# Kernel tuning notes

Hardware: AMD Instinct MI355X
Metric: run time of the kernel (lower is better)

Reference implementation:

```python
import jax, jax.numpy as jnp
import numpy as np

N_NODES = 100000


def gcn_conv(x, W, b, src, dst, n):
    # PyG GCNConv: linear transform, add self-loops, symmetric degree normalization,
    # scatter-add aggregation from src -> dst, then bias.
    h = x @ W  # [N, F_out]
    loop = jnp.arange(n, dtype=src.dtype)
    s = jnp.concatenate([src, loop])  # sources incl. self-loops
    d = jnp.concatenate([dst, loop])  # targets incl. self-loops
    deg = jax.ops.segment_sum(jnp.ones_like(d, dtype=h.dtype), d, num_segments=n)
    dinv = jnp.where(deg > 0, jax.lax.rsqrt(deg), 0.0)
    norm = dinv[s] * dinv[d]  # [E+N]
    msg = h[s] * norm[:, None]  # gather + scale
    out = jax.ops.segment_sum(msg, d, num_segments=n)  # scatter-add
    return out + b


def setup_inputs() -> dict:
    key = jax.random.key(0)
    k1, k2, k3, k4 = jax.random.split(key, 4)
    n, e = N_NODES, 1600000
    z = jax.random.normal(k1, (n, 64), dtype=jnp.float32)
    edge_index = jax.random.randint(k2, (2, e), 0, n, dtype=jnp.int64)
    # Glorot-ish init for weights, zero bias (PyG default bias init is zeros)
    W1 = jax.random.normal(k3, (64, 128), dtype=jnp.float32) * (1.0 / np.sqrt(64))
    b1 = jnp.zeros((128,), dtype=jnp.float32)
    W2 = jax.random.normal(k4, (128, 64), dtype=jnp.float32) * (1.0 / np.sqrt(128))
    b2 = jnp.zeros((64,), dtype=jnp.float32)
    return {"z": z, "edge_index": edge_index, "W1": W1, "b1": b1, "W2": W2, "b2": b2}


def reference(z, edge_index, W1, b1, W2, b2):
    n = z.shape[0]
    src, dst = edge_index[0], edge_index[1]
    h = gcn_conv(z, W1, b1, src, dst, n)
    h = jax.nn.relu(h)
    x_hat = gcn_conv(h, W2, b2, src, dst, n)
    return x_hat
```

## Files before the change

### kernel.cpp

```cpp
#include <hip/hip_runtime.h>
#include <hip/hip_bf16.h>


#define WAVE 64
#define BSHIFT 8
#define NPB 256
#define CAP 5120
#define CH 4096
#define NBMAX 512

typedef __attribute__((ext_vector_type(8))) short bf16x8;
typedef __attribute__((ext_vector_type(4))) float f32x4;

__device__ inline float bf16_to_f32(unsigned short h) {
    return __uint_as_float(((unsigned int)h) << 16);
}
__device__ inline unsigned short f32_to_bf16(float f) {
    unsigned int x = __float_as_uint(f);
    return (unsigned short)((x + 0x7FFFu + ((x >> 16) & 1u)) >> 16);
}

__global__ void prep(const float* __restrict__ W1, const float* __restrict__ W2,
                     unsigned short* __restrict__ W1t, unsigned short* __restrict__ W2t,
                     int* __restrict__ bcursor, int NB)
{
    int i = blockIdx.x * blockDim.x + threadIdx.x;
    if (i < NB) bcursor[i] = 0;
    if (i < 128 * 64) {
        int n = i >> 6, k = i & 63;
        W1t[i] = f32_to_bf16(W1[k * 128 + n]);
    }
    if (i < 64 * 128) {
        int n = i >> 7, k = i & 127;
        W2t[i] = f32_to_bf16(W2[k * 64 + n]);
    }
}

__global__ __launch_bounds__(256) void bin_edges(
        const int* __restrict__ src, const int* __restrict__ dst,
        int* __restrict__ bcursor, int2* __restrict__ ebuf, int E, int NB)
{
    __shared__ int hist[NBMAX];
    __shared__ int cur[NBMAX];
    const int t  = threadIdx.x;
    const int e0 = blockIdx.x * CH;

    for (int b = t; b < NB; b += 256) hist[b] = 0;
    __syncthreads();

#pragma unroll
    for (int j = 0; j < CH / 256; ++j) {
        int e = e0 + j * 256 + t;
        if (e < E) atomicAdd(&hist[dst[e] >> BSHIFT], 1);
    }
    __syncthreads();

    for (int b = t; b < NB; b += 256) {
        int c = hist[b];
        cur[b] = (c > 0) ? atomicAdd(&bcursor[b], c) : 0;
    }
    __syncthreads();

#pragma unroll
    for (int j = 0; j < CH / 256; ++j) {
        int e = e0 + j * 256 + t;
        if (e < E) {
            int s = src[e], d = dst[e];
            int b = d >> BSHIFT;
            int pos = atomicAdd(&cur[b], 1);
            ebuf[(size_t)b * CAP + pos] = make_int2(s, d);
        }
    }
}

__global__ __launch_bounds__(256) void build_csr(
        const int2* __restrict__ ebuf, const int* __restrict__ bcursor,
        const float* __restrict__ z, float* __restrict__ dinv,
        int* __restrict__ rbeg, int* __restrict__ rend,
        int* __restrict__ csr, unsigned short* __restrict__ u, int N)
{
    __shared__ int   h[NPB];
    __shared__ int   tmp[NPB];
    __shared__ float sdv[NPB];
    const int t   = threadIdx.x;
    const int b   = blockIdx.x;
    const int n0  = b << BSHIFT;
    const int cnt = bcursor[b];
    const size_t base = (size_t)b * CAP;

    h[t] = 0;
    __syncthreads();

    for (int i = t; i < cnt; i += 256)
        atomicAdd(&h[ebuf[base + i].y - n0], 1);
    __syncthreads();

    int deg = h[t];
    tmp[t] = deg;
    __syncthreads();
    for (int off = 1; off < 256; off <<= 1) {
        int x = (t >= off) ? tmp[t - off] : 0;
        __syncthreads();
        tmp[t] += x;
        __syncthreads();
    }
    int st = tmp[t] - deg;

    int node = n0 + t;
    float di = rsqrtf((float)deg + 1.0f);
    sdv[t] = di;
    if (node < N) {
        dinv[node] = di;
        rbeg[node] = (int)base + st;
        rend[node] = (int)base + st + deg;
    }
    h[t] = st;
    __syncthreads();

    for (int i = t; i < cnt; i += 256) {
        int2 e = ebuf[base + i];
        int p = atomicAdd(&h[e.y - n0], 1);
        csr[base + p] = e.x;
    }

    const int nloc = (N - n0 < NPB) ? (N - n0) : NPB;
    for (int i = t; i < nloc * 16; i += 256) {
        int r = i >> 4, kq = i & 15;
        float d2 = sdv[r];
        float4 v = ((const float4*)(z + (size_t)(n0 + r) * 64))[kq];
        ushort4 o;
        o.x = f32_to_bf16(v.x * d2);
        o.y = f32_to_bf16(v.y * d2);
        o.z = f32_to_bf16(v.z * d2);
        o.w = f32_to_bf16(v.w * d2);
        ((ushort4*)(u + (size_t)(n0 + r) * 64))[kq] = o;
    }
}

template<bool POST>
__global__ __launch_bounds__(256) void aggregate64_bf16(
        const unsigned short* __restrict__ hs, const int* __restrict__ rbeg,
        const int* __restrict__ rend, const int* __restrict__ csr,
        const float* __restrict__ dinv, const float* __restrict__ b,
        void* __restrict__ out_, int N)
{
    int node = (int)((blockIdx.x * (size_t)blockDim.x + threadIdx.x) >> 6);
    int lane = threadIdx.x & 63;
    if (node >= N) return;
    node = __builtin_amdgcn_readfirstlane(node);

    const int beg = rbeg[node];
    const int end = rend[node];

    float acc = bf16_to_f32(hs[(size_t)node * 64 + lane]);

    int e = beg;
    for (; e + 16 <= end; e += 16) {
        int s[16];
#pragma unroll
        for (int j = 0; j < 16; ++j) s[j] = csr[e + j];
        float v[16];
#pragma unroll
        for (int j = 0; j < 16; ++j) v[j] = bf16_to_f32(hs[(size_t)s[j] * 64 + lane]);
        float t0 = ((v[0] + v[1]) + (v[2] + v[3])) + ((v[4] + v[5]) + (v[6] + v[7]));
        float t1 = ((v[8] + v[9]) + (v[10] + v[11])) + ((v[12] + v[13]) + (v[14] + v[15]));
        acc += t0 + t1;
    }
    for (; e + 4 <= end; e += 4) {
        int s0 = csr[e+0], s1 = csr[e+1], s2 = csr[e+2], s3 = csr[e+3];
        float v0 = bf16_to_f32(hs[(size_t)s0 * 64 + lane]);
        float v1 = bf16_to_f32(hs[(size_t)s1 * 64 + lane]);
        float v2 = bf16_to_f32(hs[(size_t)s2 * 64 + lane]);
        float v3 = bf16_to_f32(hs[(size_t)s3 * 64 + lane]);
        acc += (v0 + v1) + (v2 + v3);
    }
    for (; e < end; ++e)
        acc += bf16_to_f32(hs[(size_t)csr[e] * 64 + lane]);

    if (POST) {
        float o = dinv[node] * acc + b[lane];
        ((float*)out_)[(size_t)node * 64 + lane] = o;
    } else {
        ((unsigned short*)out_)[(size_t)node * 64 + lane] = f32_to_bf16(acc);
    }
}

#define TILE 32
#define W1T_ST 72
#define W2T_ST 136
#define A_ST   72
#define X1_ST  136

__global__ __launch_bounds__(256) void gemm12_mfma(
        const unsigned short* __restrict__ agg1,
        const unsigned short* __restrict__ W1t,
        const float* __restrict__ b1,
        const unsigned short* __restrict__ W2t,
        const float* __restrict__ dinv,
        unsigned short* __restrict__ hs2, int N)
{
    __shared__ unsigned short sW1[128 * W1T_ST];
    __shared__ unsigned short sW2[64 * W2T_ST];
    __shared__ unsigned short sA[TILE * A_ST];
    __shared__ unsigned short sX[TILE * X1_ST];
    __shared__ float sdv[TILE];

    const int tid  = threadIdx.x;
    const int row0 = blockIdx.x * TILE;
    const int lane = tid & 63;
    const int wv   = tid >> 6;
    const int l16  = lane & 15;
    const int quad = lane >> 4;

    for (int i = tid; i < 128 * 8; i += 256) {
        int r = i >> 3, c = i & 7;
        *(uint4*)&sW1[r * W1T_ST + c * 8] = *(const uint4*)&W1t[r * 64 + c * 8];
    }
    for (int i = tid; i < 64 * 16; i += 256) {
        int r = i >> 4, c = i & 15;
        *(uint4*)&sW2[r * W2T_ST + c * 8] = *(const uint4*)&W2t[r * 128 + c * 8];
    }
    for (int i = tid; i < TILE * 8; i += 256) {
        int r = i >> 3, c = i & 7;
        int gr = row0 + r;
        uint4 v = make_uint4(0u, 0u, 0u, 0u);
        if (gr < N) v = *(const uint4*)&agg1[(size_t)gr * 64 + c * 8];
        *(uint4*)&sA[r * A_ST + c * 8] = v;
    }
    if (tid < TILE) {
        int gr = row0 + tid;
        sdv[tid] = (gr < N) ? dinv[gr] : 0.0f;
    }
    __syncthreads();

    {
        const int mt  = wv & 1;
        const int ntb = (wv >> 1) * 4;
        f32x4 acc[4];
#pragma unroll
        for (int t = 0; t < 4; ++t) acc[t] = (f32x4)0.0f;

#pragma unroll
        for (int k0 = 0; k0 < 64; k0 += 32) {
            bf16x8 af = *(const bf16x8*)&sA[(mt * 16 + l16) * A_ST + k0 + quad * 8];
#pragma unroll
            for (int t = 0; t < 4; ++t) {
                bf16x8 bf = *(const bf16x8*)&sW1[((ntb + t) * 16 + l16) * W1T_ST + k0 + quad * 8];
                acc[t] = __builtin_amdgcn_mfma_f32_16x16x32_bf16(af, bf, acc[t], 0, 0, 0);
            }
        }

#pragma unroll
        for (int t = 0; t < 4; ++t) {
            int col = (ntb + t) * 16 + l16;
            float bb = b1[col];
#pragma unroll
            for (int r = 0; r < 4; ++r) {
                int lr = mt * 16 + quad * 4 + r;
                float o = fmaxf(acc[t][r] * sdv[lr] + bb, 0.0f);
                sX[lr * X1_ST + col] = f32_to_bf16(o);
            }
        }
    }
    __syncthreads();

    {
        const int mt  = wv & 1;
        const int ntb = (wv >> 1) * 2;
        f32x4 acc[2];
#pragma unroll
        for (int t = 0; t < 2; ++t) acc[t] = (f32x4)0.0f;

#pragma unroll
        for (int k0 = 0; k0 < 128; k0 += 32) {
            bf16x8 af = *(const bf16x8*)&sX[(mt * 16 + l16) * X1_ST + k0 + quad * 8];
#pragma unroll
            for (int t = 0; t < 2; ++t) {
                bf16x8 bf = *(const bf16x8*)&sW2[((ntb + t) * 16 + l16) * W2T_ST + k0 + quad * 8];
                acc[t] = __builtin_amdgcn_mfma_f32_16x16x32_bf16(af, bf, acc[t], 0, 0, 0);
            }
        }

#pragma unroll
        for (int t = 0; t < 2; ++t) {
            int col = (ntb + t) * 16 + l16;
#pragma unroll
            for (int r = 0; r < 4; ++r) {
                int lr = mt * 16 + quad * 4 + r;
                int gr = row0 + lr;
                if (gr < N)
                    hs2[(size_t)gr * 64 + col] = f32_to_bf16(acc[t][r] * sdv[lr]);
            }
        }
    }
}

static inline size_t align_up(size_t x, size_t a) { return (x + a - 1) / a * a; }

extern "C" void kernel_launch(void* const* d_in, const int* in_sizes, int n_in,
                              void* d_out, int out_size, void* d_ws, size_t ws_size,
                              hipStream_t stream) {
    const float* z    = (const float*)d_in[0];
    const int*   eidx = (const int*)d_in[1];
    const float* W1   = (const float*)d_in[2];
    const float* b1   = (const float*)d_in[3];
    const float* W2   = (const float*)d_in[4];
    const float* b2   = (const float*)d_in[5];
    float* out = (float*)d_out;

    const int N = in_sizes[0] / 64;
    const int E = in_sizes[1] / 2;
    const int* src = eidx;
    const int* dst = eidx + E;
    const int NB = (N + NPB - 1) >> BSHIFT;

    char* ws = (char*)d_ws;
    size_t off = 0;
    float* dinv    = (float*)(ws + off); off = align_up(off + (size_t)N * 4, 512);
    int*   rbeg    = (int*)  (ws + off); off = align_up(off + (size_t)N * 4, 512);
    int*   rend    = (int*)  (ws + off); off = align_up(off + (size_t)N * 4, 512);
    int*   bcursor = (int*)  (ws + off); off = align_up(off + (size_t)NBMAX * 4, 512);
    unsigned short* W1t = (unsigned short*)(ws + off); off = align_up(off + 8192 * 2, 512);
    unsigned short* W2t = (unsigned short*)(ws + off); off = align_up(off + 8192 * 2, 512);
    int*   csr     = (int*)  (ws + off); off = align_up(off + (size_t)NB * CAP * 4, 512);
    float* bufA    = (float*)(ws + off); off = align_up(off + (size_t)N * 64 * 4, 512);
    float* bufB    = (float*)(ws + off); off = align_up(off + (size_t)N * 64 * 4, 512);
    float* bufC    = (float*)(ws + off); off = align_up(off + (size_t)N * 128 * 4, 512);
    int2*  ebuf    = (int2*)bufC;
    (void)ws_size;

    unsigned short* u    = (unsigned short*)bufA;
    unsigned short* agg1 = (unsigned short*)bufB;
    unsigned short* hs2  = (unsigned short*)bufA;

    prep<<<32, 256, 0, stream>>>(W1, W2, W1t, W2t, bcursor, NB);

    bin_edges<<<(E + CH - 1) / CH, 256, 0, stream>>>(src, dst, bcursor, ebuf, E, NB);
    build_csr<<<NB, 256, 0, stream>>>(ebuf, bcursor, z, dinv, rbeg, rend, csr, u, N);

    aggregate64_bf16<false><<<(N + 3) / 4, 256, 0, stream>>>(u, rbeg, rend, csr, dinv, nullptr, agg1, N);

    gemm12_mfma<<<(N + TILE - 1) / TILE, 256, 0, stream>>>(agg1, W1t, b1, W2t, dinv, hs2, N);

    aggregate64_bf16<true><<<(N + 3) / 4, 256, 0, stream>>>(hs2, rbeg, rend, csr, dinv, b2, out, N);
}
```

Before: 237.3 us.

## Fuse first-layer aggregation into the MFMA GEMM kernel and read weights from global

The first neighbor aggregation is moved into the GEMM kernel: each wave aggregates 8 nodes straight into shared memory before the two MFMA GEMMs. This removes a launch and the round trip of the intermediate agg1 buffer. Weight staging into LDS is dropped, so B fragments are read directly from global/L2. The trade-off is lower aggregation parallelism, since each block handles 32 nodes serially per wave, and possibly slower uncached weight reads.

```diff
diff --git a/kernel.cpp b/kernel.cpp
--- a/kernel.cpp
+++ b/kernel.cpp
@@ -137,12 +137,11 @@
     }
 }
 
-template<bool POST>
-__global__ __launch_bounds__(256) void aggregate64_bf16(
+__global__ __launch_bounds__(256) void aggregate64_post(
         const unsigned short* __restrict__ hs, const int* __restrict__ rbeg,
         const int* __restrict__ rend, const int* __restrict__ csr,
         const float* __restrict__ dinv, const float* __restrict__ b,
-        void* __restrict__ out_, int N)
+        float* __restrict__ out, int N)
 {
     int node = (int)((blockIdx.x * (size_t)blockDim.x + threadIdx.x) >> 6);
     int lane = threadIdx.x & 63;
@@ -177,30 +176,22 @@
     for (; e < end; ++e)
         acc += bf16_to_f32(hs[(size_t)csr[e] * 64 + lane]);
 
-    if (POST) {
-        float o = dinv[node] * acc + b[lane];
-        ((float*)out_)[(size_t)node * 64 + lane] = o;
-    } else {
-        ((unsigned short*)out_)[(size_t)node * 64 + lane] = f32_to_bf16(acc);
-    }
+    out[(size_t)node * 64 + lane] = dinv[node] * acc + b[lane];
 }
 
 #define TILE 32
-#define W1T_ST 72
-#define W2T_ST 136
 #define A_ST   72
 #define X1_ST  136
 
-__global__ __launch_bounds__(256) void gemm12_mfma(
-        const unsigned short* __restrict__ agg1,
+__global__ __launch_bounds__(256) void agg_gemm12(
+        const unsigned short* __restrict__ u,
+        const int* __restrict__ rbeg, const int* __restrict__ rend,
+        const int* __restrict__ csr, const float* __restrict__ dinv,
         const unsigned short* __restrict__ W1t,
         const float* __restrict__ b1,
         const unsigned short* __restrict__ W2t,
-        const float* __restrict__ dinv,
         unsigned short* __restrict__ hs2, int N)
 {
-    __shared__ unsigned short sW1[128 * W1T_ST];
-    __shared__ unsigned short sW2[64 * W2T_ST];
     __shared__ unsigned short sA[TILE * A_ST];
     __shared__ unsigned short sX[TILE * X1_ST];
     __shared__ float sdv[TILE];
@@ -212,24 +203,41 @@
     const int l16  = lane & 15;
     const int quad = lane >> 4;
 
-    for (int i = tid; i < 128 * 8; i += 256) {
-        int r = i >> 3, c = i & 7;
-        *(uint4*)&sW1[r * W1T_ST + c * 8] = *(const uint4*)&W1t[r * 64 + c * 8];
-    }
-    for (int i = tid; i < 64 * 16; i += 256) {
-        int r = i >> 4, c = i & 15;
-        *(uint4*)&sW2[r * W2T_ST + c * 8] = *(const uint4*)&W2t[r * 128 + c * 8];
-    }
-    for (int i = tid; i < TILE * 8; i += 256) {
-        int r = i >> 3, c = i & 7;
-        int gr = row0 + r;
-        uint4 v = make_uint4(0u, 0u, 0u, 0u);
-        if (gr < N) v = *(const uint4*)&agg1[(size_t)gr * 64 + c * 8];
-        *(uint4*)&sA[r * A_ST + c * 8] = v;
-    }
-    if (tid < TILE) {
-        int gr = row0 + tid;
-        sdv[tid] = (gr < N) ? dinv[gr] : 0.0f;
+    for (int i = 0; i < 8; ++i) {
+        const int lr   = wv * 8 + i;
+        const int node = row0 + lr;
+        float acc = 0.0f;
+        float di  = 0.0f;
+        if (node < N) {
+            di  = dinv[node];
+            acc = bf16_to_f32(u[(size_t)node * 64 + lane]);
+            const int beg = rbeg[node];
+            const int end = rend[node];
+            int e = beg;
+            for (; e + 16 <= end; e += 16) {
+                int s[16];
+#pragma unroll
+                for (int j = 0; j < 16; ++j) s[j] = csr[e + j];
+                float v[16];
+#pragma unroll
+                for (int j = 0; j < 16; ++j) v[j] = bf16_to_f32(u[(size_t)s[j] * 64 + lane]);
+                float t0 = ((v[0] + v[1]) + (v[2] + v[3])) + ((v[4] + v[5]) + (v[6] + v[7]));
+                float t1 = ((v[8] + v[9]) + (v[10] + v[11])) + ((v[12] + v[13]) + (v[14] + v[15]));
+                acc += t0 + t1;
+            }
+            for (; e + 4 <= end; e += 4) {
+                int s0 = csr[e+0], s1 = csr[e+1], s2 = csr[e+2], s3 = csr[e+3];
+                float v0 = bf16_to_f32(u[(size_t)s0 * 64 + lane]);
+                float v1 = bf16_to_f32(u[(size_t)s1 * 64 + lane]);
+                float v2 = bf16_to_f32(u[(size_t)s2 * 64 + lane]);
+                float v3 = bf16_to_f32(u[(size_t)s3 * 64 + lane]);
+                acc += (v0 + v1) + (v2 + v3);
+            }
+            for (; e < end; ++e)
+                acc += bf16_to_f32(u[(size_t)csr[e] * 64 + lane]);
+        }
+        sA[lr * A_ST + lane] = f32_to_bf16(acc);
+        if (lane == 0) sdv[lr] = di;
     }
     __syncthreads();
 
@@ -245,7 +253,8 @@
             bf16x8 af = *(const bf16x8*)&sA[(mt * 16 + l16) * A_ST + k0 + quad * 8];
 #pragma unroll
             for (int t = 0; t < 4; ++t) {
-                bf16x8 bf = *(const bf16x8*)&sW1[((ntb + t) * 16 + l16) * W1T_ST + k0 + quad * 8];
+                int ng = (ntb + t) * 16 + l16;
+                bf16x8 bf = *(const bf16x8*)&W1t[ng * 64 + k0 + quad * 8];
                 acc[t] = __builtin_amdgcn_mfma_f32_16x16x32_bf16(af, bf, acc[t], 0, 0, 0);
             }
         }
@@ -276,7 +285,8 @@
             bf16x8 af = *(const bf16x8*)&sX[(mt * 16 + l16) * X1_ST + k0 + quad * 8];
 #pragma unroll
             for (int t = 0; t < 2; ++t) {
-                bf16x8 bf = *(const bf16x8*)&sW2[((ntb + t) * 16 + l16) * W2T_ST + k0 + quad * 8];
+                int ng = (ntb + t) * 16 + l16;
+                bf16x8 bf = *(const bf16x8*)&W2t[ng * 128 + k0 + quad * 8];
                 acc[t] = __builtin_amdgcn_mfma_f32_16x16x32_bf16(af, bf, acc[t], 0, 0, 0);
             }
         }
@@ -329,18 +339,16 @@
     int2*  ebuf    = (int2*)bufC;
     (void)ws_size;
 
-    unsigned short* u    = (unsigned short*)bufA;
-    unsigned short* agg1 = (unsigned short*)bufB;
-    unsigned short* hs2  = (unsigned short*)bufA;
+    unsigned short* u   = (unsigned short*)bufA;
+    unsigned short* hs2 = (unsigned short*)bufB;
 
     prep<<<32, 256, 0, stream>>>(W1, W2, W1t, W2t, bcursor, NB);
 
     bin_edges<<<(E + CH - 1) / CH, 256, 0, stream>>>(src, dst, bcursor, ebuf, E, NB);
     build_csr<<<NB, 256, 0, stream>>>(ebuf, bcursor, z, dinv, rbeg, rend, csr, u, N);
 
-    aggregate64_bf16<false><<<(N + 3) / 4, 256, 0, stream>>>(u, rbeg, rend, csr, dinv, nullptr, agg1, N);
-
-    gemm12_mfma<<<(N + TILE - 1) / TILE, 256, 0, stream>>>(agg1, W1t, b1, W2t, dinv, hs2, N);
-
-    aggregate64_bf16<true><<<(N + 3) / 4, 256, 0, stream>>>(hs2, rbeg, rend, csr, dinv, b2, out, N);
-}
+    agg_gemm12<<<(N + TILE - 1) / TILE, 256, 0, stream>>>(
+        u, rbeg, rend, csr, dinv, W1t, b1, W2t, hs2, N);
+
+    aggregate64_post<<<(N + 3) / 4, 256, 0, stream>>>(hs2, rbeg, rend, csr, dinv, b2, out, N);
+}
```

Measured after the change: 268.4 us. 13.1% more time.

## Fuse all GCN stages into one cooperative persistent kernel with grid syncs

Applied to the files above, without the earlier changes.

Replaces the six separate launches (prep, binning, CSR build, two aggregations, fused GEMM) with a single cooperative kernel that runs each stage in grid-stride loops separated by grid-wide barriers. This removes launch gaps between kernels. The aggregation now splits each wave into two half-waves that handle two nodes, each lane loading packed bf16 pairs. The GEMM reads weights directly from global memory instead of staging them in shared memory. The risks are grid-sync overhead, lower occupancy from a persistent grid, and uncached weight reads from global memory; the buffers are also reassigned so agg1 overlays the ebuf space.

```diff
diff --git a/kernel.cpp b/kernel.cpp
--- a/kernel.cpp
+++ b/kernel.cpp
@@ -1,295 +1,311 @@
 #include <hip/hip_runtime.h>
+#include <hip/hip_cooperative_groups.h>
 #include <hip/hip_bf16.h>
 
-
-#define WAVE 64
+namespace cg = cooperative_groups;
+
+
 #define BSHIFT 8
 #define NPB 256
 #define CAP 5120
 #define CH 4096
 #define NBMAX 512
+#define TILE 32
+#define A_ST 72
+#define X1_ST 136
 
 typedef __attribute__((ext_vector_type(8))) short bf16x8;
 typedef __attribute__((ext_vector_type(4))) float f32x4;
 
-__device__ inline float bf16_to_f32(unsigned short h) {
-    return __uint_as_float(((unsigned int)h) << 16);
-}
+__device__ inline float bflo(unsigned int v) { return __uint_as_float(v << 16); }
+__device__ inline float bfhi(unsigned int v) { return __uint_as_float(v & 0xFFFF0000u); }
 __device__ inline unsigned short f32_to_bf16(float f) {
     unsigned int x = __float_as_uint(f);
     return (unsigned short)((x + 0x7FFFu + ((x >> 16) & 1u)) >> 16);
 }
 
-__global__ void prep(const float* __restrict__ W1, const float* __restrict__ W2,
-                     unsigned short* __restrict__ W1t, unsigned short* __restrict__ W2t,
-                     int* __restrict__ bcursor, int NB)
-{
-    int i = blockIdx.x * blockDim.x + threadIdx.x;
-    if (i < NB) bcursor[i] = 0;
-    if (i < 128 * 64) {
-        int n = i >> 6, k = i & 63;
-        W1t[i] = f32_to_bf16(W1[k * 128 + n]);
-    }
-    if (i < 64 * 128) {
-        int n = i >> 7, k = i & 127;
-        W2t[i] = f32_to_bf16(W2[k * 64 + n]);
-    }
-}
-
-__global__ __launch_bounds__(256) void bin_edges(
-        const int* __restrict__ src, const int* __restrict__ dst,
-        int* __restrict__ bcursor, int2* __restrict__ ebuf, int E, int NB)
-{
-    __shared__ int hist[NBMAX];
-    __shared__ int cur[NBMAX];
-    const int t  = threadIdx.x;
-    const int e0 = blockIdx.x * CH;
-
-    for (int b = t; b < NB; b += 256) hist[b] = 0;
-    __syncthreads();
-
-#pragma unroll
-    for (int j = 0; j < CH / 256; ++j) {
-        int e = e0 + j * 256 + t;
-        if (e < E) atomicAdd(&hist[dst[e] >> BSHIFT], 1);
-    }
-    __syncthreads();
-
-    for (int b = t; b < NB; b += 256) {
-        int c = hist[b];
-        cur[b] = (c > 0) ? atomicAdd(&bcursor[b], c) : 0;
-    }
-    __syncthreads();
-
-#pragma unroll
-    for (int j = 0; j < CH / 256; ++j) {
-        int e = e0 + j * 256 + t;
-        if (e < E) {
-            int s = src[e], d = dst[e];
-            int b = d >> BSHIFT;
-            int pos = atomicAdd(&cur[b], 1);
-            ebuf[(size_t)b * CAP + pos] = make_int2(s, d);
-        }
-    }
-}
-
-__global__ __launch_bounds__(256) void build_csr(
-        const int2* __restrict__ ebuf, const int* __restrict__ bcursor,
-        const float* __restrict__ z, float* __restrict__ dinv,
-        int* __restrict__ rbeg, int* __restrict__ rend,
-        int* __restrict__ csr, unsigned short* __restrict__ u, int N)
-{
-    __shared__ int   h[NPB];
-    __shared__ int   tmp[NPB];
-    __shared__ float sdv[NPB];
-    const int t   = threadIdx.x;
-    const int b   = blockIdx.x;
-    const int n0  = b << BSHIFT;
-    const int cnt = bcursor[b];
-    const size_t base = (size_t)b * CAP;
-
-    h[t] = 0;
-    __syncthreads();
-
-    for (int i = t; i < cnt; i += 256)
-        atomicAdd(&h[ebuf[base + i].y - n0], 1);
-    __syncthreads();
-
-    int deg = h[t];
-    tmp[t] = deg;
-    __syncthreads();
-    for (int off = 1; off < 256; off <<= 1) {
-        int x = (t >= off) ? tmp[t - off] : 0;
-        __syncthreads();
-        tmp[t] += x;
-        __syncthreads();
-    }
-    int st = tmp[t] - deg;
-
-    int node = n0 + t;
-    float di = rsqrtf((float)deg + 1.0f);
-    sdv[t] = di;
-    if (node < N) {
-        dinv[node] = di;
-        rbeg[node] = (int)base + st;
-        rend[node] = (int)base + st + deg;
-    }
-    h[t] = st;
-    __syncthreads();
-
-    for (int i = t; i < cnt; i += 256) {
-        int2 e = ebuf[base + i];
-        int p = atomicAdd(&h[e.y - n0], 1);
-        csr[base + p] = e.x;
-    }
-
-    const int nloc = (N - n0 < NPB) ? (N - n0) : NPB;
-    for (int i = t; i < nloc * 16; i += 256) {
-        int r = i >> 4, kq = i & 15;
-        float d2 = sdv[r];
-        float4 v = ((const float4*)(z + (size_t)(n0 + r) * 64))[kq];
-        ushort4 o;
-        o.x = f32_to_bf16(v.x * d2);
-        o.y = f32_to_bf16(v.y * d2);
-        o.z = f32_to_bf16(v.z * d2);
-        o.w = f32_to_bf16(v.w * d2);
-        ((ushort4*)(u + (size_t)(n0 + r) * 64))[kq] = o;
-    }
-}
-
-template<bool POST>
-__global__ __launch_bounds__(256) void aggregate64_bf16(
-        const unsigned short* __restrict__ hs, const int* __restrict__ rbeg,
-        const int* __restrict__ rend, const int* __restrict__ csr,
-        const float* __restrict__ dinv, const float* __restrict__ b,
-        void* __restrict__ out_, int N)
-{
-    int node = (int)((blockIdx.x * (size_t)blockDim.x + threadIdx.x) >> 6);
-    int lane = threadIdx.x & 63;
-    if (node >= N) return;
-    node = __builtin_amdgcn_readfirstlane(node);
-
-    const int beg = rbeg[node];
-    const int end = rend[node];
-
-    float acc = bf16_to_f32(hs[(size_t)node * 64 + lane]);
-
-    int e = beg;
-    for (; e + 16 <= end; e += 16) {
-        int s[16];
-#pragma unroll
-        for (int j = 0; j < 16; ++j) s[j] = csr[e + j];
-        float v[16];
-#pragma unroll
-        for (int j = 0; j < 16; ++j) v[j] = bf16_to_f32(hs[(size_t)s[j] * 64 + lane]);
-        float t0 = ((v[0] + v[1]) + (v[2] + v[3])) + ((v[4] + v[5]) + (v[6] + v[7]));
-        float t1 = ((v[8] + v[9]) + (v[10] + v[11])) + ((v[12] + v[13]) + (v[14] + v[15]));
-        acc += t0 + t1;
-    }
-    for (; e + 4 <= end; e += 4) {
-        int s0 = csr[e+0], s1 = csr[e+1], s2 = csr[e+2], s3 = csr[e+3];
-        float v0 = bf16_to_f32(hs[(size_t)s0 * 64 + lane]);
-        float v1 = bf16_to_f32(hs[(size_t)s1 * 64 + lane]);
-        float v2 = bf16_to_f32(hs[(size_t)s2 * 64 + lane]);
-        float v3 = bf16_to_f32(hs[(size_t)s3 * 64 + lane]);
-        acc += (v0 + v1) + (v2 + v3);
-    }
-    for (; e < end; ++e)
-        acc += bf16_to_f32(hs[(size_t)csr[e] * 64 + lane]);
-
-    if (POST) {
-        float o = dinv[node] * acc + b[lane];
-        ((float*)out_)[(size_t)node * 64 + lane] = o;
-    } else {
-        ((unsigned short*)out_)[(size_t)node * 64 + lane] = f32_to_bf16(acc);
-    }
-}
-
-#define TILE 32
-#define W1T_ST 72
-#define W2T_ST 136
-#define A_ST   72
-#define X1_ST  136
-
-__global__ __launch_bounds__(256) void gemm12_mfma(
-        const unsigned short* __restrict__ agg1,
-        const unsigned short* __restrict__ W1t,
-        const float* __restrict__ b1,
-        const unsigned short* __restrict__ W2t,
-        const float* __restrict__ dinv,
-        unsigned short* __restrict__ hs2, int N)
-{
-    __shared__ unsigned short sW1[128 * W1T_ST];
-    __shared__ unsigned short sW2[64 * W2T_ST];
-    __shared__ unsigned short sA[TILE * A_ST];
-    __shared__ unsigned short sX[TILE * X1_ST];
-    __shared__ float sdv[TILE];
-
-    const int tid  = threadIdx.x;
-    const int row0 = blockIdx.x * TILE;
-    const int lane = tid & 63;
-    const int wv   = tid >> 6;
-    const int l16  = lane & 15;
-    const int quad = lane >> 4;
-
-    for (int i = tid; i < 128 * 8; i += 256) {
-        int r = i >> 3, c = i & 7;
-        *(uint4*)&sW1[r * W1T_ST + c * 8] = *(const uint4*)&W1t[r * 64 + c * 8];
-    }
-    for (int i = tid; i < 64 * 16; i += 256) {
-        int r = i >> 4, c = i & 15;
-        *(uint4*)&sW2[r * W2T_ST + c * 8] = *(const uint4*)&W2t[r * 128 + c * 8];
-    }
-    for (int i = tid; i < TILE * 8; i += 256) {
-        int r = i >> 3, c = i & 7;
-        int gr = row0 + r;
-        uint4 v = make_uint4(0u, 0u, 0u, 0u);
-        if (gr < N) v = *(const uint4*)&agg1[(size_t)gr * 64 + c * 8];
-        *(uint4*)&sA[r * A_ST + c * 8] = v;
-    }
-    if (tid < TILE) {
-        int gr = row0 + tid;
-        sdv[tid] = (gr < N) ? dinv[gr] : 0.0f;
-    }
-    __syncthreads();
+struct GcnParams {
+    const float* z; const int* src; const int* dst;
+    const float* W1; const float* b1; const float* W2; const float* b2;
+    float* out;
+    float* dinv; int* rbeg; int* rend; int* bcursor;
+    unsigned short* W1t; unsigned short* W2t;
+    int* csr; int2* ebuf;
+    unsigned short* u; unsigned short* agg1; unsigned short* hs2;
+    int N, E, NB;
+};
+
+union Smem {
+    struct { int hist[NBMAX]; int cur[NBMAX]; } bin;
+    struct { int h[NPB]; int tmp[NPB]; float sdv[NPB]; } bc;
+    struct { unsigned short sA[TILE*A_ST]; unsigned short sX[TILE*X1_ST];
+             float sdv[TILE]; } gm;
+};
+
+__global__ __launch_bounds__(256, 4) void gcn_mega(GcnParams p) {
+    cg::grid_group grd = cg::this_grid();
+    __shared__ Smem sm;
+    const int tid = threadIdx.x;
+    const int gsz = gridDim.x;
+
+    for (int i = blockIdx.x * 256 + tid; i < 8192; i += gsz * 256) {
+        if (i < p.NB) p.bcursor[i] = 0;
+        { int n = i >> 6, k = i & 63;  p.W1t[i] = f32_to_bf16(p.W1[k * 128 + n]); }
+        { int n = i >> 7, k = i & 127; p.W2t[i] = f32_to_bf16(p.W2[k * 64 + n]); }
+    }
+    grd.sync();
+
+    const int nchunks = (p.E + CH - 1) / CH;
+    for (int c = blockIdx.x; c < nchunks; c += gsz) {
+        __syncthreads();
+        for (int b = tid; b < p.NB; b += 256) sm.bin.hist[b] = 0;
+        __syncthreads();
+        const int e0 = c * CH;
+#pragma unroll
+        for (int j = 0; j < CH / 256; ++j) {
+            int e = e0 + j * 256 + tid;
+            if (e < p.E) atomicAdd(&sm.bin.hist[p.dst[e] >> BSHIFT], 1);
+        }
+        __syncthreads();
+        for (int b = tid; b < p.NB; b += 256) {
+            int cc = sm.bin.hist[b];
+            sm.bin.cur[b] = (cc > 0) ? atomicAdd(&p.bcursor[b], cc) : 0;
+        }
+        __syncthreads();
+#pragma unroll
+        for (int j = 0; j < CH / 256; ++j) {
+            int e = e0 + j * 256 + tid;
+            if (e < p.E) {
+                int s = p.src[e], d = p.dst[e];
+                int b = d >> BSHIFT;
+                int pos = atomicAdd(&sm.bin.cur[b], 1);
+                p.ebuf[(size_t)b * CAP + pos] = make_int2(s, d);
+            }
+        }
+    }
+    grd.sync();
+
+    for (int b = blockIdx.x; b < p.NB; b += gsz) {
+        __syncthreads();
+        const int n0  = b << BSHIFT;
+        const int cnt = p.bcursor[b];
+        const size_t base = (size_t)b * CAP;
+        sm.bc.h[tid] = 0;
+        __syncthreads();
+        for (int i = tid; i < cnt; i += 256)
+            atomicAdd(&sm.bc.h[p.ebuf[base + i].y - n0], 1);
+        __syncthreads();
+        int deg = sm.bc.h[tid];
+        sm.bc.tmp[tid] = deg;
+        __syncthreads();
+        for (int off = 1; off < 256; off <<= 1) {
+            int x = (tid >= off) ? sm.bc.tmp[tid - off] : 0;
+            __syncthreads();
+            sm.bc.tmp[tid] += x;
+            __syncthreads();
+        }
+        int st = sm.bc.tmp[tid] - deg;
+        int node = n0 + tid;
+        float di = rsqrtf((float)deg + 1.0f);
+        sm.bc.sdv[tid] = di;
+        if (node < p.N) {
+            p.dinv[node] = di;
+            p.rbeg[node] = (int)base + st;
+            p.rend[node] = (int)base + st + deg;
+        }
+        sm.bc.h[tid] = st;
+        __syncthreads();
+        for (int i = tid; i < cnt; i += 256) {
+            int2 e = p.ebuf[base + i];
+            int pos = atomicAdd(&sm.bc.h[e.y - n0], 1);
+            p.csr[base + pos] = e.x;
+        }
+        const int nloc = (p.N - n0 < NPB) ? (p.N - n0) : NPB;
+        for (int i = tid; i < nloc * 16; i += 256) {
+            int r = i >> 4, kq = i & 15;
+            float d2 = sm.bc.sdv[r];
+            float4 v = ((const float4*)(p.z + (size_t)(n0 + r) * 64))[kq];
+            ushort4 o;
+            o.x = f32_to_bf16(v.x * d2); o.y = f32_to_bf16(v.y * d2);
+            o.z = f32_to_bf16(v.z * d2); o.w = f32_to_bf16(v.w * d2);
+            ((ushort4*)(p.u + (size_t)(n0 + r) * 64))[kq] = o;
+        }
+    }
+    grd.sync();
 
     {
-        const int mt  = wv & 1;
-        const int ntb = (wv >> 1) * 4;
-        f32x4 acc[4];
-#pragma unroll
-        for (int t = 0; t < 4; ++t) acc[t] = (f32x4)0.0f;
-
-#pragma unroll
-        for (int k0 = 0; k0 < 64; k0 += 32) {
-            bf16x8 af = *(const bf16x8*)&sA[(mt * 16 + l16) * A_ST + k0 + quad * 8];
-#pragma unroll
-            for (int t = 0; t < 4; ++t) {
-                bf16x8 bf = *(const bf16x8*)&sW1[((ntb + t) * 16 + l16) * W1T_ST + k0 + quad * 8];
-                acc[t] = __builtin_amdgcn_mfma_f32_16x16x32_bf16(af, bf, acc[t], 0, 0, 0);
-            }
-        }
-
-#pragma unroll
-        for (int t = 0; t < 4; ++t) {
-            int col = (ntb + t) * 16 + l16;
-            float bb = b1[col];
-#pragma unroll
-            for (int r = 0; r < 4; ++r) {
-                int lr = mt * 16 + quad * 4 + r;
-                float o = fmaxf(acc[t][r] * sdv[lr] + bb, 0.0f);
-                sX[lr * X1_ST + col] = f32_to_bf16(o);
-            }
-        }
-    }
-    __syncthreads();
+        const int wid  = (blockIdx.x * 256 + tid) >> 6;
+        const int nw   = (gsz * 256) >> 6;
+        const int half = (tid >> 5) & 1;
+        const int f0   = (tid & 31) * 2;
+        const int npairs = (p.N + 1) >> 1;
+        for (int pp = wid; pp < npairs; pp += nw) {
+            const int node = pp * 2 + half;
+            float ax = 0.f, ay = 0.f;
+            int e = 0, end = 0;
+            if (node < p.N) {
+                unsigned int sv = *(const unsigned int*)(p.u + (size_t)node * 64 + f0);
+                ax = bflo(sv); ay = bfhi(sv);
+                e = p.rbeg[node]; end = p.rend[node];
+            }
+            for (; e + 16 <= end; e += 16) {
+                int s[16];
+#pragma unroll
+                for (int j = 0; j < 16; ++j) s[j] = p.csr[e + j];
+                unsigned int v[16];
+#pragma unroll
+                for (int j = 0; j < 16; ++j)
+                    v[j] = *(const unsigned int*)(p.u + (size_t)s[j] * 64 + f0);
+#pragma unroll
+                for (int j = 0; j < 16; ++j) { ax += bflo(v[j]); ay += bfhi(v[j]); }
+            }
+            for (; e + 4 <= end; e += 4) {
+                int s0 = p.csr[e+0], s1 = p.csr[e+1], s2 = p.csr[e+2], s3 = p.csr[e+3];
+                unsigned int v0 = *(const unsigned int*)(p.u + (size_t)s0 * 64 + f0);
+                unsigned int v1 = *(const unsigned int*)(p.u + (size_t)s1 * 64 + f0);
+                unsigned int v2 = *(const unsigned int*)(p.u + (size_t)s2 * 64 + f0);
+                unsigned int v3 = *(const unsigned int*)(p.u + (size_t)s3 * 64 + f0);
+                ax += (bflo(v0) + bflo(v1)) + (bflo(v2) + bflo(v3));
+                ay += (bfhi(v0) + bfhi(v1)) + (bfhi(v2) + bfhi(v3));
+            }
+            for (; e < end; ++e) {
+                unsigned int v = *(const unsigned int*)(p.u + (size_t)p.csr[e] * 64 + f0);
+                ax += bflo(v); ay += bfhi(v);
+            }
+            if (node < p.N) {
+                unsigned int o = (unsigned int)f32_to_bf16(ax)
+                               | ((unsigned int)f32_to_bf16(ay) << 16);
+                *(unsigned int*)(p.agg1 + (size_t)node * 64 + f0) = o;
+            }
+        }
+    }
+    grd.sync();
 
     {
-        const int mt  = wv & 1;
-        const int ntb = (wv >> 1) * 2;
-        f32x4 acc[2];
-#pragma unroll
-        for (int t = 0; t < 2; ++t) acc[t] = (f32x4)0.0f;
-
-#pragma unroll
-        for (int k0 = 0; k0 < 128; k0 += 32) {
-            bf16x8 af = *(const bf16x8*)&sX[(mt * 16 + l16) * X1_ST + k0 + quad * 8];
-#pragma unroll
-            for (int t = 0; t < 2; ++t) {
-                bf16x8 bf = *(const bf16x8*)&sW2[((ntb + t) * 16 + l16) * W2T_ST + k0 + quad * 8];
-                acc[t] = __builtin_amdgcn_mfma_f32_16x16x32_bf16(af, bf, acc[t], 0, 0, 0);
-            }
-        }
-
-#pragma unroll
-        for (int t = 0; t < 2; ++t) {
-            int col = (ntb + t) * 16 + l16;
-#pragma unroll
-            for (int r = 0; r < 4; ++r) {
-                int lr = mt * 16 + quad * 4 + r;
-                int gr = row0 + lr;
-                if (gr < N)
-                    hs2[(size_t)gr * 64 + col] = f32_to_bf16(acc[t][r] * sdv[lr]);
+        const int lane = tid & 63, wv = tid >> 6;
+        const int l16 = lane & 15, quad = lane >> 4;
+        const int ntiles = (p.N + TILE - 1) / TILE;
+        for (int t0 = blockIdx.x; t0 < ntiles; t0 += gsz) {
+            __syncthreads();
+            const int row0 = t0 * TILE;
+            for (int i = tid; i < TILE * 8; i += 256) {
+                int r = i >> 3, c = i & 7;
+                int gr = row0 + r;
+                uint4 v = make_uint4(0u, 0u, 0u, 0u);
+                if (gr < p.N) v = *(const uint4*)(p.agg1 + (size_t)gr * 64 + c * 8);
+                *(uint4*)&sm.gm.sA[r * A_ST + c * 8] = v;
+            }
+            if (tid < TILE) {
+                int gr = row0 + tid;
+                sm.gm.sdv[tid] = (gr < p.N) ? p.dinv[gr] : 0.0f;
+            }
+            __syncthreads();
+
+            {
+                const int mt = wv & 1, ntb = (wv >> 1) * 4;
+                f32x4 acc[4];
+#pragma unroll
+                for (int t = 0; t < 4; ++t) acc[t] = (f32x4)0.0f;
+#pragma unroll
+                for (int k0 = 0; k0 < 64; k0 += 32) {
+                    bf16x8 af = *(const bf16x8*)&sm.gm.sA[(mt*16 + l16) * A_ST + k0 + quad*8];
+#pragma unroll
+                    for (int t = 0; t < 4; ++t) {
+                        int ng = (ntb + t) * 16 + l16;
+                        bf16x8 bf = *(const bf16x8*)&p.W1t[ng * 64 + k0 + quad*8];
+                        acc[t] = __builtin_amdgcn_mfma_f32_16x16x32_bf16(af, bf, acc[t], 0, 0, 0);
+                    }
+                }
+#pragma unroll
+                for (int t = 0; t < 4; ++t) {
+                    int col = (ntb + t) * 16 + l16;
+                    float bb = p.b1[col];
+#pragma unroll
+                    for (int r = 0; r < 4; ++r) {
+                        int lr = mt * 16 + quad * 4 + r;
+                        float o = fmaxf(acc[t][r] * sm.gm.sdv[lr] + bb, 0.0f);
+                        sm.gm.sX[lr * X1_ST + col] = f32_to_bf16(o);
+                    }
+                }
+            }
+            __syncthreads();
+
+            {
+                const int mt = wv & 1, ntb = (wv >> 1) * 2;
+                f32x4 acc[2];
+#pragma unroll
+                for (int t = 0; t < 2; ++t) acc[t] = (f32x4)0.0f;
+#pragma unroll
+                for (int k0 = 0; k0 < 128; k0 += 32) {
+                    bf16x8 af = *(const bf16x8*)&sm.gm.sX[(mt*16 + l16) * X1_ST + k0 + quad*8];
+#pragma unroll
+                    for (int t = 0; t < 2; ++t) {
+                        int ng = (ntb + t) * 16 + l16;
+                        bf16x8 bf = *(const bf16x8*)&p.W2t[ng * 128 + k0 + quad*8];
+                        acc[t] = __builtin_amdgcn_mfma_f32_16x16x32_bf16(af, bf, acc[t], 0, 0, 0);
+                    }
+                }
+#pragma unroll
+                for (int t = 0; t < 2; ++t) {
+                    int col = (ntb + t) * 16 + l16;
+#pragma unroll
+                    for (int r = 0; r < 4; ++r) {
+                        int lr = mt * 16 + quad * 4 + r;
+                        int gr = row0 + lr;
+                        if (gr < p.N)
+                            p.hs2[(size_t)gr * 64 + col] = f32_to_bf16(acc[t][r] * sm.gm.sdv[lr]);
+                    }
+                }
+            }
+        }
+    }
+    grd.sync();
+
+    {
+        const int wid  = (blockIdx.x * 256 + tid) >> 6;
+        const int nw   = (gsz * 256) >> 6;
+        const int half = (tid >> 5) & 1;
+        const int f0   = (tid & 31) * 2;
+        const int npairs = (p.N + 1) >> 1;
+        for (int pp = wid; pp < npairs; pp += nw) {
+            const int node = pp * 2 + half;
+            float ax = 0.f, ay = 0.f;
+            int e = 0, end = 0;
+            if (node < p.N) {
+                unsigned int sv = *(const unsigned int*)(p.hs2 + (size_t)node * 64 + f0);
+                ax = bflo(sv); ay = bfhi(sv);
+                e = p.rbeg[node]; end = p.rend[node];
+            }
+            for (; e + 16 <= end; e += 16) {
+                int s[16];
+#pragma unroll
+                for (int j = 0; j < 16; ++j) s[j] = p.csr[e + j];
+                unsigned int v[16];
+#pragma unroll
+                for (int j = 0; j < 16; ++j)
+                    v[j] = *(const unsigned int*)(p.hs2 + (size_t)s[j] * 64 + f0);
+#pragma unroll
+                for (int j = 0; j < 16; ++j) { ax += bflo(v[j]); ay += bfhi(v[j]); }
+            }
+            for (; e + 4 <= end; e += 4) {
+                int s0 = p.csr[e+0], s1 = p.csr[e+1], s2 = p.csr[e+2], s3 = p.csr[e+3];
+                unsigned int v0 = *(const unsigned int*)(p.hs2 + (size_t)s0 * 64 + f0);
+                unsigned int v1 = *(const unsigned int*)(p.hs2 + (size_t)s1 * 64 + f0);
+                unsigned int v2 = *(const unsigned int*)(p.hs2 + (size_t)s2 * 64 + f0);
+                unsigned int v3 = *(const unsigned int*)(p.hs2 + (size_t)s3 * 64 + f0);
+                ax += (bflo(v0) + bflo(v1)) + (bflo(v2) + bflo(v3));
+                ay += (bfhi(v0) + bfhi(v1)) + (bfhi(v2) + bfhi(v3));
+            }
+            for (; e < end; ++e) {
+                unsigned int v = *(const unsigned int*)(p.hs2 + (size_t)p.csr[e] * 64 + f0);
+                ax += bflo(v); ay += bfhi(v);
+            }
+            if (node < p.N) {
+                float di = p.dinv[node];
+                float2 o;
+                o.x = di * ax + p.b2[f0];
+                o.y = di * ay + p.b2[f0 + 1];
+                *(float2*)(p.out + (size_t)node * 64 + f0) = o;
             }
         }
     }
@@ -306,12 +322,9 @@
     const float* b1   = (const float*)d_in[3];
     const float* W2   = (const float*)d_in[4];
     const float* b2   = (const float*)d_in[5];
-    float* out = (float*)d_out;
 
     const int N = in_sizes[0] / 64;
     const int E = in_sizes[1] / 2;
-    const int* src = eidx;
-    const int* dst = eidx + E;
     const int NB = (N + NPB - 1) >> BSHIFT;
 
     char* ws = (char*)d_ws;
@@ -326,21 +339,28 @@
     float* bufA    = (float*)(ws + off); off = align_up(off + (size_t)N * 64 * 4, 512);
     float* bufB    = (float*)(ws + off); off = align_up(off + (size_t)N * 64 * 4, 512);
     float* bufC    = (float*)(ws + off); off = align_up(off + (size_t)N * 128 * 4, 512);
-    int2*  ebuf    = (int2*)bufC;
     (void)ws_size;
 
-    unsigned short* u    = (unsigned short*)bufA;
-    unsigned short* agg1 = (unsigned short*)bufB;
-    unsigned short* hs2  = (unsigned short*)bufA;
-
-    prep<<<32, 256, 0, stream>>>(W1, W2, W1t, W2t, bcursor, NB);
-
-    bin_edges<<<(E + CH - 1) / CH, 256, 0, stream>>>(src, dst, bcursor, ebuf, E, NB);
-    build_csr<<<NB, 256, 0, stream>>>(ebuf, bcursor, z, dinv, rbeg, rend, csr, u, N);
-
-    aggregate64_bf16<false><<<(N + 3) / 4, 256, 0, stream>>>(u, rbeg, rend, csr, dinv, nullptr, agg1, N);
-
-    gemm12_mfma<<<(N + TILE - 1) / TILE, 256, 0, stream>>>(agg1, W1t, b1, W2t, dinv, hs2, N);
-
-    aggregate64_bf16<true><<<(N + 3) / 4, 256, 0, stream>>>(hs2, rbeg, rend, csr, dinv, b2, out, N);
+    GcnParams prm;
+    prm.z = z; prm.src = eidx; prm.dst = eidx + E;
+    prm.W1 = W1; prm.b1 = b1; prm.W2 = W2; prm.b2 = b2;
+    prm.out = (float*)d_out;
+    prm.dinv = dinv; prm.rbeg = rbeg; prm.rend = rend; prm.bcursor = bcursor;
+    prm.W1t = W1t; prm.W2t = W2t;
+    prm.csr = csr; prm.ebuf = (int2*)bufC;
+    prm.u = (unsigned short*)bufA;
+    prm.agg1 = (unsigned short*)bufC;
+    prm.hs2 = (unsigned short*)bufB;
+    prm.N = N; prm.E = E; prm.NB = NB;
+
+    int dev = 0;
+    hipGetDevice(&dev);
+    int nCU = 256;
+    hipDeviceGetAttribute(&nCU, hipDeviceAttributeMultiprocessorCount, dev);
+    int maxB = 0;
+    hipOccupancyMaxActiveBlocksPerMultiprocessor(&maxB, gcn_mega, 256, 0);
+    int bpc = maxB < 1 ? 1 : (maxB > 8 ? 8 : maxB);
+
+    void* args[] = { &prm };
+    hipLaunchCooperativeKernel(gcn_mega, dim3(nCU * bpc), dim3(256), args, 0, stream);
 }
```

After: 649.8 us. 2.74x slower.
